# Optimization experiments

Hardware: AMD Instinct MI355X
Metric: run time of the kernel (lower is better)

## Reference

```python
import jax, jax.numpy as jnp
import numpy as np

NUM_HEADS = 4
HEAD_DIM = 64  # out_dim // num_heads = 256 // 4
NEG_SLOPE = 0.2


def setup_inputs() -> dict:
    key = jax.random.key(0)
    k1, k2 = jax.random.split(key)
    h = jax.random.normal(k1, (8, 2048, 256), dtype=jnp.float32)
    # Linear(in_dim, head_dim*num_heads, bias=False): store as [in_dim, out_dim]
    W = jax.random.normal(k2, (256, 256), dtype=jnp.float32) * (1.0 / np.sqrt(256.0))
    return {"h": h, "W": W}


def reference(h, W):
    B, T, _ = h.shape
    # Wh: (B, H, T, D)
    Wh = (h @ W).reshape(B, T, NUM_HEADS, HEAD_DIM).transpose(0, 2, 1, 3)
    scale = 1.0 / (HEAD_DIM ** 0.5)
    # full T x T scores per head, LeakyReLU then softmax over keys
    scores = jnp.einsum('bhtd,bhsd->bhts', Wh, Wh) * scale
    attention = jax.nn.softmax(jax.nn.leaky_relu(scores, negative_slope=NEG_SLOPE), axis=-1)
    h_prime = jnp.einsum('bhts,bhsd->bhtd', attention, Wh)
    # concat=True: (B, T, H*D)
    return h_prime.transpose(0, 2, 1, 3).reshape(B, T, NUM_HEADS * HEAD_DIM)
```

## Files before the change

kernel.cpp:

```cpp
#include <hip/hip_runtime.h>

#define T_SEQ 2048
#define NH 4
#define DH 64

typedef __bf16 bf16x8 __attribute__((ext_vector_type(8)));
typedef float f32x4 __attribute__((ext_vector_type(4)));
typedef unsigned short u16x8 __attribute__((ext_vector_type(8)));

__device__ __forceinline__ unsigned short f2bf_rne(float x) {
  unsigned int u = __builtin_bit_cast(unsigned int, x);
  u += 0x7fffu + ((u >> 16) & 1u);
  return (unsigned short)(u >> 16);
}
__device__ __forceinline__ float bf2f(unsigned short s) {
  unsigned int u = ((unsigned int)s) << 16;
  return __builtin_bit_cast(float, u);
}

__global__ void prep_w(const float* __restrict__ W,
                       unsigned short* __restrict__ WtHi,
                       unsigned short* __restrict__ WtLo) {
  __shared__ float ls[32][65];
  const int tid = threadIdx.x;
  const int k0 = (blockIdx.x >> 2) * 32;
  const int n0 = (blockIdx.x & 3) * 64;
#pragma unroll
  for (int i = 0; i < 8; i++) {
    int e = i * 256 + tid;
    int r = e >> 6, c = e & 63;
    ls[r][c] = W[(k0 + r) * 256 + n0 + c];
  }
  __syncthreads();
  const int n = tid & 63;
  const int part = tid >> 6;
  u16x8 vh, vl;
#pragma unroll
  for (int j = 0; j < 8; j++) {
    float w = ls[part * 8 + j][n];
    unsigned short h16 = f2bf_rne(w);
    vh[j] = h16;
    vl[j] = f2bf_rne(w - bf2f(h16));
  }
  size_t dst = (size_t)(n0 + n) * 256 + k0 + part * 8;
  *(u16x8*)&WtHi[dst] = vh;
  *(u16x8*)&WtLo[dst] = vl;
}

__global__ __launch_bounds__(256, 2) void wh_gemm(
    const float* __restrict__ h,
    const unsigned short* __restrict__ WtHi,
    const unsigned short* __restrict__ WtLo,
    unsigned short* __restrict__ Kb, unsigned short* __restrict__ Vt) {
  __shared__ __align__(16) unsigned short ktile[32][264];
  __shared__ __align__(16) unsigned short vtile[256][40];
  const int tid = threadIdx.x;
  const int wave = tid >> 6, lane = tid & 63, l15 = lane & 15, quad = lane >> 4;
  const int m0b = blockIdx.x * 32;
  const int m0 = m0b + (wave & 1) * 16;
  const int n0w = (wave >> 1) * 128;
  f32x4 acc[8];
#pragma unroll
  for (int nt = 0; nt < 8; nt++) acc[nt] = (f32x4){0.f, 0.f, 0.f, 0.f};

  for (int kc = 0; kc < 8; kc++) {
    const float4* hp = (const float4*)&h[(size_t)(m0 + l15) * 256 + kc * 32 + quad * 8];
    float4 a0 = hp[0], a1 = hp[1];
    float xs[8] = {a0.x, a0.y, a0.z, a0.w, a1.x, a1.y, a1.z, a1.w};
    u16x8 ah, al;
#pragma unroll
    for (int j = 0; j < 8; j++) {
      unsigned short h16 = f2bf_rne(xs[j]);
      ah[j] = h16;
      al[j] = f2bf_rne(xs[j] - bf2f(h16));
    }
    bf16x8 ahi = __builtin_bit_cast(bf16x8, ah);
    bf16x8 alo = __builtin_bit_cast(bf16x8, al);
#pragma unroll
    for (int nt = 0; nt < 8; nt++) {
      size_t wb = (size_t)(n0w + nt * 16 + l15) * 256 + kc * 32 + quad * 8;
      bf16x8 bhi = *(const bf16x8*)&WtHi[wb];
      bf16x8 blo = *(const bf16x8*)&WtLo[wb];
      acc[nt] = __builtin_amdgcn_mfma_f32_16x16x32_bf16(ahi, bhi, acc[nt], 0, 0, 0);
      acc[nt] = __builtin_amdgcn_mfma_f32_16x16x32_bf16(alo, bhi, acc[nt], 0, 0, 0);
      acc[nt] = __builtin_amdgcn_mfma_f32_16x16x32_bf16(ahi, blo, acc[nt], 0, 0, 0);
    }
  }
  const float s1 = 0.424664717f;
  const int tl = (wave & 1) * 16 + quad * 4;
#pragma unroll
  for (int nt = 0; nt < 8; nt++) {
    int n = n0w + nt * 16 + l15;
#pragma unroll
    for (int r = 0; r < 4; r++) {
      float v = acc[nt][r];
      ktile[tl + r][n] = f2bf_rne(v * s1);
      vtile[n][tl + r] = f2bf_rne(v);
    }
  }
  __syncthreads();
  {
    int t = tid >> 3, seg = tid & 7;
    int m = m0b + t, b = m >> 11, tt = m & 2047;
    int head = seg >> 1, d0 = (seg & 1) * 32;
    unsigned short* dst = &Kb[((size_t)(b * NH + head) * T_SEQ + tt) * DH + d0];
#pragma unroll
    for (int q = 0; q < 4; q++)
      *(u16x8*)&dst[q * 8] = *(const u16x8*)&ktile[t][seg * 32 + q * 8];
  }
  {
    int n = tid, head = n >> 6, d = n & 63;
    int b = m0b >> 11, t0 = m0b & 2047;
    unsigned short* dst = &Vt[((size_t)(b * NH + head) * DH + d) * T_SEQ + t0];
#pragma unroll
    for (int q = 0; q < 4; q++)
      *(u16x8*)&dst[q * 8] = *(const u16x8*)&vtile[n][q * 8];
  }
}

struct Frag {
  bf16x8 k[2][2];
  bf16x8 v[4];
};

__device__ __forceinline__ void load_frags(Frag& f, const unsigned short* Kbh,
                                           const unsigned short* Vbh, int s0,
                                           int l15, int quad) {
#pragma unroll
  for (int mt = 0; mt < 2; mt++)
#pragma unroll
    for (int kc = 0; kc < 2; kc++)
      f.k[mt][kc] = *(const bf16x8*)&Kbh[(size_t)(s0 + mt * 16 + l15) * DH + kc * 32 + quad * 8];
#pragma unroll
  for (int dt = 0; dt < 4; dt++)
    f.v[dt] = *(const bf16x8*)&Vbh[(size_t)(dt * 16 + l15) * T_SEQ + s0 + quad * 8];
}

__device__ __forceinline__ void step(const Frag& f, const bf16x8 bq[4][2],
                                     f32x4 o[4][4], float* lsum,
                                     unsigned short* Pw, int l15, int quad) {
  f32x4 s[2][4];
#pragma unroll
  for (int mt = 0; mt < 2; mt++)
#pragma unroll
    for (int nt = 0; nt < 4; nt++) {
      f32x4 c = {0.f, 0.f, 0.f, 0.f};
      c = __builtin_amdgcn_mfma_f32_16x16x32_bf16(f.k[mt][0], bq[nt][0], c, 0, 0, 0);
      c = __builtin_amdgcn_mfma_f32_16x16x32_bf16(f.k[mt][1], bq[nt][1], c, 0, 0, 0);
      s[mt][nt] = c;
    }
#pragma unroll
  for (int mt = 0; mt < 2; mt++)
#pragma unroll
    for (int nt = 0; nt < 4; nt++) {
      float e0, e1, e2, e3;
      {
        float v0 = s[mt][nt][0], v1 = s[mt][nt][1];
        float v2 = s[mt][nt][2], v3 = s[mt][nt][3];
        e0 = __builtin_amdgcn_exp2f(fmaxf(v0, 0.2f * v0));
        e1 = __builtin_amdgcn_exp2f(fmaxf(v1, 0.2f * v1));
        e2 = __builtin_amdgcn_exp2f(fmaxf(v2, 0.2f * v2));
        e3 = __builtin_amdgcn_exp2f(fmaxf(v3, 0.2f * v3));
      }
      lsum[nt] += (e0 + e1) + (e2 + e3);
      uint2 pk;
      pk.x = (__builtin_bit_cast(unsigned int, e1) & 0xffff0000u) |
             (__builtin_bit_cast(unsigned int, e0) >> 16);
      pk.y = (__builtin_bit_cast(unsigned int, e3) & 0xffff0000u) |
             (__builtin_bit_cast(unsigned int, e2) >> 16);
      *(uint2*)&Pw[(nt * 16 + l15) * 40 + mt * 16 + quad * 4] = pk;
    }
  __builtin_amdgcn_s_waitcnt(0xC07F);
#pragma unroll
  for (int mt = 0; mt < 4; mt++) {
    bf16x8 pa = *(const bf16x8*)&Pw[(mt * 16 + l15) * 40 + quad * 8];
#pragma unroll
    for (int dt = 0; dt < 4; dt++)
      o[mt][dt] = __builtin_amdgcn_mfma_f32_16x16x32_bf16(pa, f.v[dt], o[mt][dt], 0, 0, 0);
  }
}

__global__ __launch_bounds__(256, 1) void attn(
    const unsigned short* __restrict__ Kb, const unsigned short* __restrict__ Vt,
    float* __restrict__ out) {
  __shared__ __align__(16) unsigned short Pw_all[4][64 * 40];
  __shared__ float inv_lds[4][64];
  const int tid = threadIdx.x, wave = tid >> 6, lane = tid & 63;
  const int l15 = lane & 15, quad = lane >> 4;
  const int bh = blockIdx.x & 31;
  const int qt = blockIdx.x >> 5;
  const int q0 = qt * 256 + wave * 64;
  const unsigned short* Kbh = Kb + (size_t)bh * T_SEQ * DH;
  const unsigned short* Vbh = Vt + (size_t)bh * DH * T_SEQ;
  unsigned short* Pw = Pw_all[wave];

  bf16x8 bq[4][2];
#pragma unroll
  for (int nt = 0; nt < 4; nt++)
#pragma unroll
    for (int kc = 0; kc < 2; kc++)
      bq[nt][kc] = *(const bf16x8*)&Kbh[(size_t)(q0 + nt * 16 + l15) * DH + kc * 32 + quad * 8];

  f32x4 o[4][4];
  float lsum[4] = {0.f, 0.f, 0.f, 0.f};
#pragma unroll
  for (int mt = 0; mt < 4; mt++)
#pragma unroll
    for (int dt = 0; dt < 4; dt++) o[mt][dt] = (f32x4){0.f, 0.f, 0.f, 0.f};

  Frag fa, fb;
  load_frags(fa, Kbh, Vbh, 0, l15, quad);
  for (int it = 0; it < 64; it += 2) {
    load_frags(fb, Kbh, Vbh, (it + 1) * 32, l15, quad);
    step(fa, bq, o, lsum, Pw, l15, quad);
    load_frags(fa, Kbh, Vbh, (it + 2 < 64) ? (it + 2) * 32 : 0, l15, quad);
    step(fb, bq, o, lsum, Pw, l15, quad);
  }

#pragma unroll
  for (int nt = 0; nt < 4; nt++) {
    float l = lsum[nt];
    l += __shfl_xor(l, 16, 64);
    l += __shfl_xor(l, 32, 64);
    if (quad == 0) inv_lds[wave][nt * 16 + l15] = 1.0f / l;
  }
  __builtin_amdgcn_s_waitcnt(0xC07F);

  const int b = bh >> 2, head = bh & 3;
#pragma unroll
  for (int mt = 0; mt < 4; mt++) {
#pragma unroll
    for (int r = 0; r < 4; r++) {
      float iv = inv_lds[wave][mt * 16 + quad * 4 + r];
      int qg = q0 + mt * 16 + quad * 4 + r;
      float* dst = &out[((size_t)b * T_SEQ + qg) * 256 + head * DH];
#pragma unroll
      for (int dt = 0; dt < 4; dt++) dst[dt * 16 + l15] = o[mt][dt][r] * iv;
    }
  }
}

extern "C" void kernel_launch(void* const* d_in, const int* in_sizes, int n_in,
                              void* d_out, int out_size, void* d_ws, size_t ws_size,
                              hipStream_t stream) {
  const float* h = (const float*)d_in[0];
  const float* W = (const float*)d_in[1];
  float* out = (float*)d_out;
  unsigned short* Kb = (unsigned short*)d_ws;
  unsigned short* Vt = Kb + (size_t)32 * T_SEQ * DH;
  unsigned short* WtHi = (unsigned short*)out;
  unsigned short* WtLo = WtHi + 65536;
  prep_w<<<32, 256, 0, stream>>>(W, WtHi, WtLo);
  wh_gemm<<<512, 256, 0, stream>>>(h, WtHi, WtLo, Kb, Vt);
  attn<<<256, 256, 0, stream>>>(Kb, Vt, out);
}
```

Baseline: 171.5 us.

## Split keys across waves in attention with LDS reduction and more blocks

Attention blocks now cover 64 queries each, with the four waves each processing a quarter of the keys. Partial outputs and row sums are reduced through shared memory before the final write. This raises the grid to 1024 blocks and occupancy to 3 blocks per CU, to hide latency better. In exchange it drops the explicit fragment double-buffering and adds a reduction step with several barriers. It also pads the LDS strides for P and the K tile, and vectorizes the V-tile stores in the projection GEMM.

New measurement: 206.6 us. 1.2x slower.

```diff
diff --git a/kernel.cpp b/kernel.cpp
--- a/kernel.cpp
+++ b/kernel.cpp
@@ -3,6 +3,7 @@
 #define T_SEQ 2048
 #define NH 4
 #define DH 64
+#define PW 36
 
 typedef __bf16 bf16x8 __attribute__((ext_vector_type(8)));
 typedef float f32x4 __attribute__((ext_vector_type(4)));
@@ -52,7 +53,7 @@
     const unsigned short* __restrict__ WtHi,
     const unsigned short* __restrict__ WtLo,
     unsigned short* __restrict__ Kb, unsigned short* __restrict__ Vt) {
-  __shared__ __align__(16) unsigned short ktile[32][264];
+  __shared__ __align__(16) unsigned short ktile[32][272];
   __shared__ __align__(16) unsigned short vtile[256][40];
   const int tid = threadIdx.x;
   const int wave = tid >> 6, lane = tid & 63, l15 = lane & 15, quad = lane >> 4;
@@ -91,12 +92,14 @@
 #pragma unroll
   for (int nt = 0; nt < 8; nt++) {
     int n = n0w + nt * 16 + l15;
+    ushort4 vp;
 #pragma unroll
     for (int r = 0; r < 4; r++) {
       float v = acc[nt][r];
       ktile[tl + r][n] = f2bf_rne(v * s1);
-      vtile[n][tl + r] = f2bf_rne(v);
-    }
+      ((unsigned short*)&vp)[r] = f2bf_rne(v);
+    }
+    *(uint2*)&vtile[n][tl] = __builtin_bit_cast(uint2, vp);
   }
   __syncthreads();
   {
@@ -118,81 +121,20 @@
   }
 }
 
-struct Frag {
-  bf16x8 k[2][2];
-  bf16x8 v[4];
-};
-
-__device__ __forceinline__ void load_frags(Frag& f, const unsigned short* Kbh,
-                                           const unsigned short* Vbh, int s0,
-                                           int l15, int quad) {
-#pragma unroll
-  for (int mt = 0; mt < 2; mt++)
-#pragma unroll
-    for (int kc = 0; kc < 2; kc++)
-      f.k[mt][kc] = *(const bf16x8*)&Kbh[(size_t)(s0 + mt * 16 + l15) * DH + kc * 32 + quad * 8];
-#pragma unroll
-  for (int dt = 0; dt < 4; dt++)
-    f.v[dt] = *(const bf16x8*)&Vbh[(size_t)(dt * 16 + l15) * T_SEQ + s0 + quad * 8];
-}
-
-__device__ __forceinline__ void step(const Frag& f, const bf16x8 bq[4][2],
-                                     f32x4 o[4][4], float* lsum,
-                                     unsigned short* Pw, int l15, int quad) {
-  f32x4 s[2][4];
-#pragma unroll
-  for (int mt = 0; mt < 2; mt++)
-#pragma unroll
-    for (int nt = 0; nt < 4; nt++) {
-      f32x4 c = {0.f, 0.f, 0.f, 0.f};
-      c = __builtin_amdgcn_mfma_f32_16x16x32_bf16(f.k[mt][0], bq[nt][0], c, 0, 0, 0);
-      c = __builtin_amdgcn_mfma_f32_16x16x32_bf16(f.k[mt][1], bq[nt][1], c, 0, 0, 0);
-      s[mt][nt] = c;
-    }
-#pragma unroll
-  for (int mt = 0; mt < 2; mt++)
-#pragma unroll
-    for (int nt = 0; nt < 4; nt++) {
-      float e0, e1, e2, e3;
-      {
-        float v0 = s[mt][nt][0], v1 = s[mt][nt][1];
-        float v2 = s[mt][nt][2], v3 = s[mt][nt][3];
-        e0 = __builtin_amdgcn_exp2f(fmaxf(v0, 0.2f * v0));
-        e1 = __builtin_amdgcn_exp2f(fmaxf(v1, 0.2f * v1));
-        e2 = __builtin_amdgcn_exp2f(fmaxf(v2, 0.2f * v2));
-        e3 = __builtin_amdgcn_exp2f(fmaxf(v3, 0.2f * v3));
-      }
-      lsum[nt] += (e0 + e1) + (e2 + e3);
-      uint2 pk;
-      pk.x = (__builtin_bit_cast(unsigned int, e1) & 0xffff0000u) |
-             (__builtin_bit_cast(unsigned int, e0) >> 16);
-      pk.y = (__builtin_bit_cast(unsigned int, e3) & 0xffff0000u) |
-             (__builtin_bit_cast(unsigned int, e2) >> 16);
-      *(uint2*)&Pw[(nt * 16 + l15) * 40 + mt * 16 + quad * 4] = pk;
-    }
-  __builtin_amdgcn_s_waitcnt(0xC07F);
-#pragma unroll
-  for (int mt = 0; mt < 4; mt++) {
-    bf16x8 pa = *(const bf16x8*)&Pw[(mt * 16 + l15) * 40 + quad * 8];
-#pragma unroll
-    for (int dt = 0; dt < 4; dt++)
-      o[mt][dt] = __builtin_amdgcn_mfma_f32_16x16x32_bf16(pa, f.v[dt], o[mt][dt], 0, 0, 0);
-  }
-}
-
-__global__ __launch_bounds__(256, 1) void attn(
+__global__ __launch_bounds__(256, 3) void attn(
     const unsigned short* __restrict__ Kb, const unsigned short* __restrict__ Vt,
     float* __restrict__ out) {
-  __shared__ __align__(16) unsigned short Pw_all[4][64 * 40];
-  __shared__ float inv_lds[4][64];
+  __shared__ __align__(16) char smem[2 * 64 * 68 * 4];
+  __shared__ float lbuf[4][64];
+  __shared__ float inv_s[64];
   const int tid = threadIdx.x, wave = tid >> 6, lane = tid & 63;
   const int l15 = lane & 15, quad = lane >> 4;
   const int bh = blockIdx.x & 31;
   const int qt = blockIdx.x >> 5;
-  const int q0 = qt * 256 + wave * 64;
+  const int q0 = qt * 64;
   const unsigned short* Kbh = Kb + (size_t)bh * T_SEQ * DH;
   const unsigned short* Vbh = Vt + (size_t)bh * DH * T_SEQ;
-  unsigned short* Pw = Pw_all[wave];
+  unsigned short* Pw = (unsigned short*)smem + wave * 64 * PW;
 
   bf16x8 bq[4][2];
 #pragma unroll
@@ -208,13 +150,52 @@
 #pragma unroll
     for (int dt = 0; dt < 4; dt++) o[mt][dt] = (f32x4){0.f, 0.f, 0.f, 0.f};
 
-  Frag fa, fb;
-  load_frags(fa, Kbh, Vbh, 0, l15, quad);
-  for (int it = 0; it < 64; it += 2) {
-    load_frags(fb, Kbh, Vbh, (it + 1) * 32, l15, quad);
-    step(fa, bq, o, lsum, Pw, l15, quad);
-    load_frags(fa, Kbh, Vbh, (it + 2 < 64) ? (it + 2) * 32 : 0, l15, quad);
-    step(fb, bq, o, lsum, Pw, l15, quad);
+  int s0 = wave * 512;
+  for (int it = 0; it < 16; it++, s0 += 32) {
+    bf16x8 ka[2][2], va[4];
+#pragma unroll
+    for (int mt = 0; mt < 2; mt++)
+#pragma unroll
+      for (int kc = 0; kc < 2; kc++)
+        ka[mt][kc] = *(const bf16x8*)&Kbh[(size_t)(s0 + mt * 16 + l15) * DH + kc * 32 + quad * 8];
+#pragma unroll
+    for (int dt = 0; dt < 4; dt++)
+      va[dt] = *(const bf16x8*)&Vbh[(size_t)(dt * 16 + l15) * T_SEQ + s0 + quad * 8];
+
+#pragma unroll
+    for (int mt = 0; mt < 2; mt++) {
+#pragma unroll
+      for (int nt = 0; nt < 4; nt++) {
+        f32x4 s = {0.f, 0.f, 0.f, 0.f};
+        s = __builtin_amdgcn_mfma_f32_16x16x32_bf16(ka[mt][0], bq[nt][0], s, 0, 0, 0);
+        s = __builtin_amdgcn_mfma_f32_16x16x32_bf16(ka[mt][1], bq[nt][1], s, 0, 0, 0);
+        float v0 = s[0], v1 = s[1], v2 = s[2], v3 = s[3];
+        float e0 = __builtin_amdgcn_exp2f(fmaxf(v0, 0.2f * v0));
+        float e1 = __builtin_amdgcn_exp2f(fmaxf(v1, 0.2f * v1));
+        float e2 = __builtin_amdgcn_exp2f(fmaxf(v2, 0.2f * v2));
+        float e3 = __builtin_amdgcn_exp2f(fmaxf(v3, 0.2f * v3));
+        lsum[nt] += (e0 + e1) + (e2 + e3);
+        uint2 pk;
+        pk.x = (__builtin_bit_cast(unsigned int, e1) & 0xffff0000u) |
+               (__builtin_bit_cast(unsigned int, e0) >> 16);
+        pk.y = (__builtin_bit_cast(unsigned int, e3) & 0xffff0000u) |
+               (__builtin_bit_cast(unsigned int, e2) >> 16);
+        *(uint2*)&Pw[(nt * 16 + l15) * PW + mt * 16 + quad * 4] = pk;
+      }
+    }
+    __builtin_amdgcn_s_waitcnt(0xC07F);
+
+#pragma unroll
+    for (int mt = 0; mt < 4; mt++) {
+      const unsigned short* pr = &Pw[(mt * 16 + l15) * PW + quad * 8];
+      uint2 plo = *(const uint2*)pr;
+      uint2 phi = *(const uint2*)(pr + 4);
+      uint4 pu = {plo.x, plo.y, phi.x, phi.y};
+      bf16x8 pa = __builtin_bit_cast(bf16x8, pu);
+#pragma unroll
+      for (int dt = 0; dt < 4; dt++)
+        o[mt][dt] = __builtin_amdgcn_mfma_f32_16x16x32_bf16(pa, va[dt], o[mt][dt], 0, 0, 0);
+    }
   }
 
 #pragma unroll
@@ -222,20 +203,58 @@
     float l = lsum[nt];
     l += __shfl_xor(l, 16, 64);
     l += __shfl_xor(l, 32, 64);
-    if (quad == 0) inv_lds[wave][nt * 16 + l15] = 1.0f / l;
-  }
-  __builtin_amdgcn_s_waitcnt(0xC07F);
-
-  const int b = bh >> 2, head = bh & 3;
-#pragma unroll
-  for (int mt = 0; mt < 4; mt++) {
-#pragma unroll
-    for (int r = 0; r < 4; r++) {
-      float iv = inv_lds[wave][mt * 16 + quad * 4 + r];
-      int qg = q0 + mt * 16 + quad * 4 + r;
-      float* dst = &out[((size_t)b * T_SEQ + qg) * 256 + head * DH];
-#pragma unroll
-      for (int dt = 0; dt < 4; dt++) dst[dt * 16 + l15] = o[mt][dt][r] * iv;
+    if (quad == 0) lbuf[wave][nt * 16 + l15] = l;
+  }
+  __syncthreads();
+  float* cbuf0 = (float*)smem;
+  float* cbuf1 = cbuf0 + 64 * 68;
+  if (wave >= 2) {
+    float* cb = (wave == 2) ? cbuf0 : cbuf1;
+#pragma unroll
+    for (int mt = 0; mt < 4; mt++)
+#pragma unroll
+      for (int dt = 0; dt < 4; dt++)
+        *(f32x4*)&cb[(dt * 16 + l15) * 68 + mt * 16 + quad * 4] = o[mt][dt];
+  }
+  if (wave == 0) {
+    float s = lbuf[0][lane] + lbuf[1][lane] + lbuf[2][lane] + lbuf[3][lane];
+    inv_s[lane] = 1.0f / s;
+  }
+  __syncthreads();
+  if (wave < 2) {
+    float* cb = (wave == 0) ? cbuf0 : cbuf1;
+#pragma unroll
+    for (int mt = 0; mt < 4; mt++)
+#pragma unroll
+      for (int dt = 0; dt < 4; dt++)
+        o[mt][dt] += *(const f32x4*)&cb[(dt * 16 + l15) * 68 + mt * 16 + quad * 4];
+  }
+  __syncthreads();
+  if (wave == 1) {
+#pragma unroll
+    for (int mt = 0; mt < 4; mt++)
+#pragma unroll
+      for (int dt = 0; dt < 4; dt++)
+        *(f32x4*)&cbuf0[(dt * 16 + l15) * 68 + mt * 16 + quad * 4] = o[mt][dt];
+  }
+  __syncthreads();
+  if (wave == 0) {
+#pragma unroll
+    for (int mt = 0; mt < 4; mt++)
+#pragma unroll
+      for (int dt = 0; dt < 4; dt++)
+        o[mt][dt] += *(const f32x4*)&cbuf0[(dt * 16 + l15) * 68 + mt * 16 + quad * 4];
+    const int b = bh >> 2, head = bh & 3;
+#pragma unroll
+    for (int mt = 0; mt < 4; mt++) {
+#pragma unroll
+      for (int r = 0; r < 4; r++) {
+        int q = mt * 16 + quad * 4 + r;
+        float iv = inv_s[q];
+        float* dst = &out[((size_t)b * T_SEQ + q0 + q) * 256 + head * 64];
+#pragma unroll
+        for (int dt = 0; dt < 4; dt++) dst[dt * 16 + l15] = o[mt][dt][r] * iv;
+      }
     }
   }
 }
@@ -252,5 +271,5 @@
   unsigned short* WtLo = WtHi + 65536;
   prep_w<<<32, 256, 0, stream>>>(W, WtHi, WtLo);
   wh_gemm<<<512, 256, 0, stream>>>(h, WtHi, WtLo, Kb, Vt);
-  attn<<<256, 256, 0, stream>>>(Kb, Vt, out);
-}
+  attn<<<1024, 256, 0, stream>>>(Kb, Vt, out);
+}
```
